# Kernel optimization log

Hardware: AMD Instinct MI355X
Metric: run time of the kernel (lower is better)

The kernel has to match this reference:

```python
import jax, jax.numpy as jnp
import numpy as np

DN = ('NCHW', 'OIHW', 'NCHW')

def conv(x, w, b, stride, pad):
    y = jax.lax.conv_general_dilated(x, w, (stride, stride), [(pad, pad), (pad, pad)], dimension_numbers=DN)
    return y if b is None else y + b[None, :, None, None]

def convT(x, w, b, stride, pad):
    # torch ConvTranspose2d weight layout: (in, out, kh, kw)
    wt = jnp.flip(w, (2, 3)).transpose(1, 0, 2, 3)
    p = w.shape[2] - 1 - pad
    y = jax.lax.conv_general_dilated(x, wt, (1, 1), [(p, p), (p, p)], lhs_dilation=(stride, stride), dimension_numbers=DN)
    return y + b[None, :, None, None]

def resblock(x, wa, wb):
    h = conv(jax.nn.relu(x), wa, None, 1, 1)   # 3x3, 128->32, no bias
    h = conv(jax.nn.relu(h), wb, None, 1, 0)   # 1x1, 32->128, no bias
    return x + h

def setup_inputs() -> dict:
    key = jax.random.key(0)
    ks = jax.random.split(key, 32)
    def w(i, shape):
        fan_in = int(np.prod(shape[1:]))
        return jax.random.normal(ks[i], shape, jnp.float32) * (1.0 / np.sqrt(fan_in))
    K, D = 512, 64
    inp = {
        'x':   jax.random.normal(ks[0], (16, 1, 256, 256), jnp.float32),
        'ew1': w(1, (64, 1, 4, 4)),    'eb1': jnp.zeros((64,), jnp.float32),
        'ew2': w(2, (128, 64, 4, 4)),  'eb2': jnp.zeros((128,), jnp.float32),
        'ew3': w(3, (128, 128, 3, 3)), 'eb3': jnp.zeros((128,), jnp.float32),
        'er1a': w(4, (32, 128, 3, 3)), 'er1b': w(5, (128, 32, 1, 1)),
        'er2a': w(6, (32, 128, 3, 3)), 'er2b': w(7, (128, 32, 1, 1)),
        'pw': w(8, (64, 128, 1, 1)),   'pb': jnp.zeros((64,), jnp.float32),
        'codebook': jax.random.uniform(ks[9], (K, D), jnp.float32, -1.0 / K, 1.0 / K),
        'dw1': w(10, (128, 64, 3, 3)), 'db1': jnp.zeros((128,), jnp.float32),
        'dr1a': w(11, (32, 128, 3, 3)), 'dr1b': w(12, (128, 32, 1, 1)),
        'dr2a': w(13, (32, 128, 3, 3)), 'dr2b': w(14, (128, 32, 1, 1)),
        'dtw1': w(15, (128, 64, 4, 4)), 'dtb1': jnp.zeros((64,), jnp.float32),  # ConvT: (in,out,kh,kw)
        'dtw2': w(16, (64, 1, 4, 4)),   'dtb2': jnp.zeros((1,), jnp.float32),
    }
    return inp

def vq(z, codebook, beta=0.25):
    zn = z.transpose(0, 2, 3, 1)                 # NHWC
    flat = zn.reshape(-1, codebook.shape[1])     # [N, D]
    d = jnp.sum(flat * flat, axis=1, keepdims=True) + jnp.sum(codebook * codebook, axis=1) - 2.0 * (flat @ codebook.T)  # [N, K]
    idx = jnp.argmin(d, axis=1)
    enc = jax.nn.one_hot(idx, codebook.shape[0], dtype=z.dtype)  # [N, K]
    q = codebook[idx].reshape(zn.shape)
    e_loss = jnp.mean(jnp.square(jax.lax.stop_gradient(q) - zn))
    q_loss = jnp.mean(jnp.square(q - jax.lax.stop_gradient(zn)))
    loss = q_loss + beta * e_loss
    q_st = zn + jax.lax.stop_gradient(q - zn)    # straight-through
    avg = jnp.mean(enc, axis=0)
    perplexity = jnp.exp(-jnp.sum(avg * jnp.log(avg + 1e-10)))
    return loss, q_st.transpose(0, 3, 1, 2), perplexity, enc

def reference(x, ew1, eb1, ew2, eb2, ew3, eb3, er1a, er1b, er2a, er2b, pw, pb, codebook, dw1, db1, dr1a, dr1b, dr2a, dr2b, dtw1, dtb1, dtw2, dtb2):
    # encoder
    h = jax.nn.relu(conv(x, ew1, eb1, 2, 1))
    h = jax.nn.relu(conv(h, ew2, eb2, 2, 1))
    h = conv(h, ew3, eb3, 1, 1)
    h = resblock(h, er1a, er1b)
    h = resblock(h, er2a, er2b)
    h = jax.nn.relu(h)
    z = conv(h, pw, pb, 1, 0)
    # vector quantizer
    loss, quantized, perplexity, encodings = vq(z, codebook)
    # decoder
    d = conv(quantized, dw1, db1, 1, 1)
    d = resblock(d, dr1a, dr1b)
    d = resblock(d, dr2a, dr2b)
    d = jax.nn.relu(convT(d, dtw1, dtb1, 2, 1))
    x_rec = convT(d, dtw2, dtb2, 2, 1)
    return (loss, x_rec, perplexity, encodings, quantized)
```

## Files before the change

### kernel.cpp

```cpp
#include <hip/hip_runtime.h>

#define TPB 256

typedef __attribute__((ext_vector_type(8))) short s8v;
typedef __attribute__((ext_vector_type(4))) float f4v;
typedef __bf16 bf16x8v __attribute__((ext_vector_type(8)));

__device__ inline short f2b(float f) {
    unsigned u = __builtin_bit_cast(unsigned, f);
    unsigned r = (u + 0x7FFF + ((u >> 16) & 1)) >> 16;
    return (short)r;
}
__device__ inline float b2f(short s) {
    unsigned u = ((unsigned)(unsigned short)s) << 16;
    return __builtin_bit_cast(float, u);
}
__device__ inline f4v mfma16(s8v a, s8v b, f4v c) {
    return __builtin_amdgcn_mfma_f32_16x16x32_bf16(
        __builtin_bit_cast(bf16x8v, a), __builtin_bit_cast(bf16x8v, b), c, 0, 0, 0);
}

struct WtDesc { const float* src; int CO, CI, T, iohw, start; };
struct WtArgs { WtDesc d[13]; int total; };

__global__ __launch_bounds__(256)
void wtall_k(WtArgs a, short* dst)
{
    int i = blockIdx.x * 256 + threadIdx.x;
    if (i >= a.total) return;
    int s = 0;
    for (int j = 1; j < 13; ++j) if (i >= a.d[j].start) s = j;
    int off = i - a.d[s].start;
    int CI = a.d[s].CI, CO = a.d[s].CO, T = a.d[s].T;
    int KC = CI >> 5, NT = CO >> 4;
    int j    = off & 7;
    int lane = (off >> 3) & 63;
    int rl = lane & 15, qd = lane >> 4;
    int blk = off >> 9;
    int nt  = blk % NT;
    int rest = blk / NT;
    int kc  = rest % KC;
    int tap = rest / KC;
    int co = nt * 16 + rl;
    int ci = kc * 32 + qd * 8 + j;
    float v = a.d[s].iohw ? a.d[s].src[(ci * CO + co) * T + tap]
                          : a.d[s].src[(co * CI + ci) * T + tap];
    dst[i] = f2b(v);
}

__global__ __launch_bounds__(256)
void cbprep_k(const float* __restrict__ cb, short* __restrict__ cbh,
              short* __restrict__ cbl, float* __restrict__ cbsq)
{
    int c = blockIdx.x * 256 + threadIdx.x;
    const float* src = cb + (size_t)c * 64;
    const int nt = c >> 4, rl = c & 15;
    float sq = 0.f;
    for (int d = 0; d < 64; ++d) {
        float v = src[d];
        sq += v * v;
        short h = f2b(v);
        short lo = f2b(v - b2f(h));
        int kc = d >> 5, qd = (d >> 3) & 3, j = d & 7;
        int pos = ((kc * 32 + nt) << 9) + ((qd * 16 + rl) << 3) + j;
        cbh[pos] = h;
        cbl[pos] = lo;
    }
    cbsq[c] = sq;
}

__global__ __launch_bounds__(256)
void conv1_k(const float* __restrict__ x, const float* __restrict__ w,
             const float* __restrict__ bias, short* __restrict__ out)
{
    __shared__ float sx[4 * 256];
    const int tid = threadIdx.x;
    const int oh = blockIdx.x, n = blockIdx.y;
    const int co = tid & 63, wv = tid >> 6;

    float wr[16];
#pragma unroll
    for (int t = 0; t < 16; ++t) wr[t] = w[co * 16 + t];
    const float b = bias[co];

    const float* xp = x + (size_t)n * 65536;
    for (int e = tid; e < 1024; e += 256) {
        int kh = e >> 8, col = e & 255;
        int ih = oh * 2 - 1 + kh;
        sx[e] = ((unsigned)ih < 256u) ? xp[ih * 256 + col] : 0.f;
    }
    __syncthreads();

    short* op = out + (((size_t)n * 128 + oh) * 128) * 64 + co;
#pragma unroll 4
    for (int i = 0; i < 32; ++i) {
        int ow = wv * 32 + i;
        int iwb = ow * 2 - 1;
        float acc = b;
#pragma unroll
        for (int kh = 0; kh < 4; ++kh) {
#pragma unroll
            for (int kw = 0; kw < 4; ++kw) {
                int iw = iwb + kw;
                float v = ((unsigned)iw < 256u) ? sx[kh * 256 + iw] : 0.f;
                acc = fmaf(v, wr[kh * 4 + kw], acc);
            }
        }
        op[(size_t)ow * 64] = f2b(fmaxf(acc, 0.f));
    }
}

template<int CI, int CO, bool RELU_IN, bool RELU_OUT, bool OUT_F32>
__global__ __launch_bounds__(256)
void pconv3s_k(const short* __restrict__ in, const short* __restrict__ wt,
               const float* __restrict__ bias, void* __restrict__ outv)
{
    constexpr int KC = CI / 32, NT = CO / 16;
    constexpr int NT2 = NT / 2;
    __shared__ short sA[3 * 66 * 40];

    const int tid = threadIdx.x;
    const int oh = blockIdx.x;
    const int n  = blockIdx.y;
    const short* inb = in + (size_t)n * 4096 * CI;
    const int w = tid >> 6, l = tid & 63, rl = l & 15, qd = l >> 4;
    const int mh = w & 1, nh = w >> 1;

    f4v acc[2][NT2];
#pragma unroll
    for (int a2 = 0; a2 < 2; ++a2)
#pragma unroll
        for (int nt = 0; nt < NT2; ++nt) acc[a2][nt] = (f4v)0.f;

    for (int kc = 0; kc < KC; ++kc) {
        __syncthreads();
        for (int e = tid; e < 792; e += 256) {
            int cell = e >> 2, kcn = e & 3;
            int hr = cell / 66, col = cell - hr * 66;
            int ih = oh - 1 + hr, iw = col - 1;
            s8v v = (s8v)0;
            if ((unsigned)ih < 64u && (unsigned)iw < 64u) {
                v = *(const s8v*)(inb + ((size_t)ih * 64 + iw) * CI + kc * 32 + kcn * 8);
                if (RELU_IN) {
#pragma unroll
                    for (int j = 0; j < 8; ++j) if (v[j] < (short)0) v[j] = 0;
                }
            }
            *(s8v*)&sA[(hr * 66 + col) * 40 + kcn * 8] = v;
        }
        __syncthreads();

#pragma unroll
        for (int tap = 0; tap < 9; ++tap) {
            const int kh = tap / 3, kw = tap % 3;
            s8v af[2];
#pragma unroll
            for (int a2 = 0; a2 < 2; ++a2)
                af[a2] = *(const s8v*)&sA[(kh * 66 + mh * 32 + a2 * 16 + rl + kw) * 40 + qd * 8];
            const short* wb = wt + (((size_t)(tap * KC + kc) * NT + nh * NT2) << 9) + l * 8;
#pragma unroll
            for (int nt = 0; nt < NT2; ++nt) {
                s8v b = *(const s8v*)(wb + ((size_t)nt << 9));
#pragma unroll
                for (int a2 = 0; a2 < 2; ++a2)
                    acc[a2][nt] = mfma16(af[a2], b, acc[a2][nt]);
            }
        }
    }

#pragma unroll
    for (int a2 = 0; a2 < 2; ++a2) {
#pragma unroll
        for (int rg = 0; rg < 4; ++rg) {
            int ow = mh * 32 + a2 * 16 + qd * 4 + rg;
            size_t row = (size_t)n * 4096 + (size_t)oh * 64 + ow;
#pragma unroll
            for (int nt = 0; nt < NT2; ++nt) {
                int co = nh * NT2 * 16 + nt * 16 + rl;
                float v = acc[a2][nt][rg];
                if (bias) v += bias[co];
                if (RELU_OUT) v = fmaxf(v, 0.f);
                if (OUT_F32) ((float*)outv)[row * CO + co] = v;
                else         ((short*)outv)[row * CO + co] = f2b(v);
            }
        }
    }
}

__global__ __launch_bounds__(256)
void rfuse_k(const short* __restrict__ in, const short* __restrict__ wa,
             const short* __restrict__ wb, short* __restrict__ out)
{
    __shared__ short sA[3 * 66 * 40];
    short* sMid = sA;

    const int tid = threadIdx.x;
    const int oh = blockIdx.x;
    const int n  = blockIdx.y;
    const short* inb = in + (size_t)n * 4096 * 128;
    const int w = tid >> 6, l = tid & 63, rl = l & 15, qd = l >> 4;

    f4v acc1[2];
    acc1[0] = (f4v)0.f; acc1[1] = (f4v)0.f;

    for (int kc = 0; kc < 4; ++kc) {
        __syncthreads();
        for (int e = tid; e < 792; e += 256) {
            int cell = e >> 2, kcn = e & 3;
            int hr = cell / 66, col = cell - hr * 66;
            int ih = oh - 1 + hr, iw = col - 1;
            s8v v = (s8v)0;
            if ((unsigned)ih < 64u && (unsigned)iw < 64u) {
                v = *(const s8v*)(inb + ((size_t)ih * 64 + iw) * 128 + kc * 32 + kcn * 8);
#pragma unroll
                for (int j = 0; j < 8; ++j) if (v[j] < (short)0) v[j] = 0;
            }
            *(s8v*)&sA[(hr * 66 + col) * 40 + kcn * 8] = v;
        }
        __syncthreads();

#pragma unroll
        for (int tap = 0; tap < 9; ++tap) {
            const int kh = tap / 3, kw = tap % 3;
            s8v af = *(const s8v*)&sA[(kh * 66 + w * 16 + rl + kw) * 40 + qd * 8];
            const short* wp = wa + (((size_t)(tap * 4 + kc) * 2) << 9) + l * 8;
            acc1[0] = mfma16(af, *(const s8v*)(wp),       acc1[0]);
            acc1[1] = mfma16(af, *(const s8v*)(wp + 512), acc1[1]);
        }
    }

    __syncthreads();
#pragma unroll
    for (int nt = 0; nt < 2; ++nt)
#pragma unroll
        for (int rg = 0; rg < 4; ++rg) {
            int m  = w * 16 + qd * 4 + rg;
            int co = nt * 16 + rl;
            sMid[m * 40 + co] = f2b(fmaxf(acc1[nt][rg], 0.f));
        }
    __syncthreads();

    f4v acc2[8];
#pragma unroll
    for (int nt = 0; nt < 8; ++nt) acc2[nt] = (f4v)0.f;

    s8v am = *(const s8v*)&sMid[(w * 16 + rl) * 40 + qd * 8];
#pragma unroll
    for (int nt = 0; nt < 8; ++nt) {
        s8v b = *(const s8v*)(wb + ((size_t)nt << 9) + l * 8);
        acc2[nt] = mfma16(am, b, acc2[nt]);
    }

    short* outb = out + (size_t)n * 4096 * 128;
    const size_t sp0 = (size_t)oh * 64;
#pragma unroll
    for (int rg = 0; rg < 4; ++rg) {
        int m = w * 16 + qd * 4 + rg;
        size_t sp = sp0 + m;
#pragma unroll
        for (int nt = 0; nt < 8; ++nt) {
            int co = nt * 16 + rl;
            float v = acc2[nt][rg] + b2f(inb[sp * 128 + co]);
            outb[sp * 128 + co] = f2b(v);
        }
    }
}

template<int CI, int CO, bool RELU_IN, bool RELU_OUT, bool OUT_F32>
__global__ __launch_bounds__(256)
void pconv1s_k(const short* __restrict__ in, const short* __restrict__ wt,
               const float* __restrict__ bias, void* __restrict__ outv)
{
    constexpr int KC = CI / 32, NT = CO / 16;
    __shared__ short sA[64 * 40];

    const int tid = threadIdx.x;
    const size_t r0 = (size_t)blockIdx.x * 64;
    const int w = tid >> 6, l = tid & 63, rl = l & 15, qd = l >> 4;

    f4v acc[NT];
#pragma unroll
    for (int nt = 0; nt < NT; ++nt) acc[nt] = (f4v)0.f;

    for (int kc = 0; kc < KC; ++kc) {
        __syncthreads();
        {
            int row = tid >> 2, kcn = tid & 3;
            s8v v = *(const s8v*)(in + (r0 + row) * CI + kc * 32 + kcn * 8);
            if (RELU_IN) {
#pragma unroll
                for (int j = 0; j < 8; ++j) if (v[j] < (short)0) v[j] = 0;
            }
            *(s8v*)&sA[row * 40 + kcn * 8] = v;
        }
        __syncthreads();

        s8v af = *(const s8v*)&sA[(w * 16 + rl) * 40 + qd * 8];
        const short* wb = wt + (((size_t)kc * NT) << 9) + l * 8;
#pragma unroll
        for (int nt = 0; nt < NT; ++nt) {
            s8v b = *(const s8v*)(wb + ((size_t)nt << 9));
            acc[nt] = mfma16(af, b, acc[nt]);
        }
    }

#pragma unroll
    for (int rg = 0; rg < 4; ++rg) {
        size_t row = r0 + w * 16 + qd * 4 + rg;
#pragma unroll
        for (int nt = 0; nt < NT; ++nt) {
            int co = nt * 16 + rl;
            float v = acc[nt][rg];
            if (bias) v += bias[co];
            if (RELU_OUT) v = fmaxf(v, 0.f);
            if (OUT_F32) ((float*)outv)[row * CO + co] = v;
            else         ((short*)outv)[row * CO + co] = f2b(v);
        }
    }
}

__global__ __launch_bounds__(256)
void pconv2_k(const short* __restrict__ in, const short* __restrict__ wt,
              const float* __restrict__ bias, short* __restrict__ out)
{
    __shared__ short sA[2 * 4 * 66 * 40];
    const int tid = threadIdx.x;
    const int oh = blockIdx.x, n = blockIdx.y;
    const short* inb = in + (size_t)n * 16384 * 64;
    const int w = tid >> 6, l = tid & 63, rl = l & 15, qd = l >> 4;
    const int mh = w & 1, nh = w >> 1;

    f4v acc[2][4];
#pragma unroll
    for (int a2 = 0; a2 < 2; ++a2)
#pragma unroll
        for (int nt = 0; nt < 4; ++nt) acc[a2][nt] = (f4v)0.f;

    for (int kc = 0; kc < 2; ++kc) {
        __syncthreads();
        for (int e = tid; e < 2112; e += 256) {
            int cell = e >> 2, kcn = e & 3;
            int par = cell / 264;
            int rem = cell - par * 264;
            int hr = rem / 66, c = rem - hr * 66;
            int iw = par ? (2 * c - 1) : (2 * c);
            int ih = oh * 2 - 1 + hr;
            s8v v = (s8v)0;
            if ((unsigned)ih < 128u && (unsigned)iw < 128u)
                v = *(const s8v*)(inb + ((size_t)ih * 128 + iw) * 64 + kc * 32 + kcn * 8);
            *(s8v*)&sA[((par * 4 + hr) * 66 + c) * 40 + kcn * 8] = v;
        }
        __syncthreads();

#pragma unroll
        for (int tap = 0; tap < 16; ++tap) {
            const int kh = tap >> 2, kw = tap & 3;
            const int par = 1 - (kw & 1), cofs = kw >> 1;
            s8v af[2];
#pragma unroll
            for (int a2 = 0; a2 < 2; ++a2) {
                int ow = mh * 32 + a2 * 16 + rl;
                af[a2] = *(const s8v*)&sA[((par * 4 + kh) * 66 + ow + cofs) * 40 + qd * 8];
            }
            const short* wb = wt + (((size_t)(tap * 2 + kc) * 8 + nh * 4) << 9) + l * 8;
#pragma unroll
            for (int nt = 0; nt < 4; ++nt) {
                s8v b = *(const s8v*)(wb + ((size_t)nt << 9));
#pragma unroll
                for (int a2 = 0; a2 < 2; ++a2)
                    acc[a2][nt] = mfma16(af[a2], b, acc[a2][nt]);
            }
        }
    }

#pragma unroll
    for (int a2 = 0; a2 < 2; ++a2) {
#pragma unroll
        for (int rg = 0; rg < 4; ++rg) {
            int ow = mh * 32 + a2 * 16 + qd * 4 + rg;
            size_t row = (size_t)n * 4096 + (size_t)oh * 64 + ow;
#pragma unroll
            for (int nt = 0; nt < 4; ++nt) {
                int co = nh * 64 + nt * 16 + rl;
                float v = acc[a2][nt][rg] + bias[co];
                out[row * 128 + co] = f2b(fmaxf(v, 0.f));
            }
        }
    }
}

__global__ __launch_bounds__(256)
void pct1_k(const short* __restrict__ in, const short* __restrict__ wt,
            const float* __restrict__ bias, short* __restrict__ out)
{
    __shared__ short sA[3 * 66 * 40];
    const int tid = threadIdx.x;
    const int bx = blockIdx.x, n = blockIdx.y;
    const int P = bx & 1;
    const int q2 = bx >> 1;
    const int oh0 = (q2 >> 1) * 4 + (q2 & 1);
    const int p = (oh0 + 1) & 1;
    const int ihb0 = (oh0 + 1 - p) >> 1;
    const short* inb = in + (size_t)n * 4096 * 128;
    const int w = tid >> 6, l = tid & 63, rl = l & 15, qd = l >> 4;
    const int mh = w & 1, nh = w >> 1;

    f4v acc[4][2];
#pragma unroll
    for (int a4 = 0; a4 < 4; ++a4)
#pragma unroll
        for (int nt = 0; nt < 2; ++nt) acc[a4][nt] = (f4v)0.f;

    for (int kc = 0; kc < 4; ++kc) {
        __syncthreads();
        for (int e = tid; e < 792; e += 256) {
            int cell = e >> 2, kcn = e & 3;
            int hr = cell / 66, c = cell - hr * 66;
            int ih = ihb0 - 1 + hr, iw = c - 1;
            s8v v = (s8v)0;
            if ((unsigned)ih < 64u && (unsigned)iw < 64u)
                v = *(const s8v*)(inb + ((size_t)ih * 64 + iw) * 128 + kc * 32 + kcn * 8);
            *(s8v*)&sA[(hr * 66 + c) * 40 + kcn * 8] = v;
        }
        __syncthreads();

#pragma unroll
        for (int a = 0; a < 2; ++a)
#pragma unroll
        for (int b = 0; b < 2; ++b) {
            const int kh = p + 2 * a;
            const int kw = (1 - P) + 2 * b;
            const int tap = kh * 4 + kw;
            const int hrw = mh + 1 - a;
            s8v af[4];
#pragma unroll
            for (int a4 = 0; a4 < 4; ++a4)
                af[a4] = *(const s8v*)&sA[(hrw * 66 + a4 * 16 + rl + P - b + 1) * 40 + qd * 8];
            const short* wbp = wt + (((size_t)(tap * 4 + kc) * 4 + nh * 2) << 9) + l * 8;
#pragma unroll
            for (int nt = 0; nt < 2; ++nt) {
                s8v bb = *(const s8v*)(wbp + ((size_t)nt << 9));
#pragma unroll
                for (int a4 = 0; a4 < 4; ++a4)
                    acc[a4][nt] = mfma16(af[a4], bb, acc[a4][nt]);
            }
        }
    }

#pragma unroll
    for (int a4 = 0; a4 < 4; ++a4) {
#pragma unroll
        for (int rg = 0; rg < 4; ++rg) {
            int j = a4 * 16 + qd * 4 + rg;
            int oh = oh0 + 2 * mh, ow = 2 * j + P;
            size_t pb = (((size_t)n * 128 + oh) * 128 + ow) * 64;
#pragma unroll
            for (int nt = 0; nt < 2; ++nt) {
                int co = nh * 32 + nt * 16 + rl;
                float v = acc[a4][nt][rg] + bias[co];
                out[pb + co] = f2b(fmaxf(v, 0.f));
            }
        }
    }
}

__global__ __launch_bounds__(256)
void convt2_k(const short* __restrict__ in, const float* __restrict__ w,
              const float* __restrict__ bias, float* __restrict__ out)
{
    __shared__ float sw[16 * 64];
    const int tid = threadIdx.x;
    for (int e = tid; e < 1024; e += 256) { int ci = e >> 4, tap = e & 15; sw[tap * 64 + ci] = w[e]; }
    __syncthreads();

    const int i = blockIdx.x * 256 + tid;
    const int n = i >> 16, s = i & 65535;
    const int oh = s >> 8, ow = s & 255;

    const int p = (oh + 1) & 1, q = (ow + 1) & 1;
    const int ihb = (oh + 1 - p) >> 1, iwb = (ow + 1 - q) >> 1;

    float acc = bias[0];
#pragma unroll
    for (int a = 0; a < 2; ++a) {
        int ih = ihb - a, kh = p + 2 * a;
        bool vr = (unsigned)ih < 128u;
#pragma unroll
        for (int b = 0; b < 2; ++b) {
            int iw = iwb - b, kw = q + 2 * b;
            if (vr && (unsigned)iw < 128u) {
                const short* ip = in + (((size_t)n * 128 + ih) * 128 + iw) * 64;
                const float* wp = &sw[(kh * 4 + kw) * 64];
#pragma unroll
                for (int c = 0; c < 64; c += 8) {
                    s8v v = *(const s8v*)(ip + c);
#pragma unroll
                    for (int j = 0; j < 8; ++j) acc += b2f(v[j]) * wp[c + j];
                }
            }
        }
    }
    out[i] = acc;
}

__global__ __launch_bounds__(256)
void vqm_k(const float* __restrict__ z, const short* __restrict__ cbh,
           const short* __restrict__ cbl, const float* __restrict__ cbsq,
           const float* __restrict__ cb,
           float* __restrict__ quant, short* __restrict__ qb,
           int* __restrict__ idxp, float* __restrict__ errbuf)
{
    __shared__ float zs[64 * 68];
    __shared__ short scb[2][8192];
    __shared__ int sidx[64];
    __shared__ float serr[4];
    float* qc = (float*)&scb[0][0];

    const int tid = threadIdx.x;
    const int w = tid >> 6, l = tid & 63, rl = l & 15, qd = l >> 4;
    const int r0 = blockIdx.x * 64;

    for (int e = tid; e < 1024; e += 256) {
        int row = e >> 4, c4 = e & 15;
        float4 t = ((const float4*)(z + (size_t)(r0 + row) * 64))[c4];
        *(float4*)&zs[row * 68 + c4 * 4] = t;
    }
    __syncthreads();

    s8v zh[2], zl[2];
#pragma unroll
    for (int kc = 0; kc < 2; ++kc) {
        const float* zp = &zs[(w * 16 + rl) * 68 + kc * 32 + qd * 8];
        s8v hi, lo;
#pragma unroll
        for (int j = 0; j < 8; ++j) {
            float v = zp[j];
            short h = f2b(v);
            hi[j] = h;
            lo[j] = f2b(v - b2f(h));
        }
        zh[kc] = hi; zl[kc] = lo;
    }

    float best[4]; int bidx[4];
#pragma unroll
    for (int rg = 0; rg < 4; ++rg) { best[rg] = 3.4e38f; bidx[rg] = 0; }

    for (int ch = 0; ch < 4; ++ch) {
        __syncthreads();
        for (int e = tid; e < 1024; e += 256) {
            int kcL = e >> 9, rest = e & 511;
            int ntl = rest >> 6, off = rest & 63;
            int srcIdx = (kcL * 32 + ch * 8 + ntl) * 64 + off;
            *(s8v*)&scb[0][e * 8] = ((const s8v*)cbh)[srcIdx];
            *(s8v*)&scb[1][e * 8] = ((const s8v*)cbl)[srcIdx];
        }
        __syncthreads();

        float sq[8];
#pragma unroll
        for (int nt = 0; nt < 8; ++nt) sq[nt] = cbsq[ch * 128 + nt * 16 + rl];

        f4v acc[8];
#pragma unroll
        for (int nt = 0; nt < 8; ++nt) acc[nt] = (f4v)0.f;
#pragma unroll
        for (int kc = 0; kc < 2; ++kc) {
#pragma unroll
            for (int nt = 0; nt < 8; ++nt) {
                s8v bh = *(const s8v*)&scb[0][(kc * 8 + nt) * 512 + l * 8];
                s8v bl = *(const s8v*)&scb[1][(kc * 8 + nt) * 512 + l * 8];
                acc[nt] = mfma16(zh[kc], bh, acc[nt]);
                acc[nt] = mfma16(zh[kc], bl, acc[nt]);
                acc[nt] = mfma16(zl[kc], bh, acc[nt]);
            }
        }

#pragma unroll
        for (int rg = 0; rg < 4; ++rg) {
            float bd = best[rg]; int bi = bidx[rg];
#pragma unroll
            for (int nt = 0; nt < 8; ++nt) {
                float d = sq[nt] - 2.f * acc[nt][rg];
                int code = ch * 128 + nt * 16 + rl;
                if (d < bd) { bd = d; bi = code; }
            }
            best[rg] = bd; bidx[rg] = bi;
        }
    }

#pragma unroll
    for (int rg = 0; rg < 4; ++rg) {
        float bd = best[rg]; int bi = bidx[rg];
#pragma unroll
        for (int off = 1; off < 16; off <<= 1) {
            float od = __shfl_xor(bd, off, 64);
            int   oi = __shfl_xor(bi, off, 64);
            if (od < bd || (od == bd && oi < bi)) { bd = od; bi = oi; }
        }
        if (rl == 0) sidx[w * 16 + qd * 4 + rg] = bi;
    }
    __syncthreads();

    const int n = r0 >> 12, s0 = r0 & 4095;
    float err = 0.f;
#pragma unroll 4
    for (int i = 0; i < 16; ++i) {
        int rr = w * 16 + i;
        int bi = sidx[rr];
        float c = cb[(size_t)bi * 64 + l];
        float zv = zs[rr * 68 + l];
        float dd = zv - c;
        err += dd * dd;
        qb[(size_t)(r0 + rr) * 64 + l] = f2b(c);
        qc[l * 68 + rr] = c;
    }
#pragma unroll
    for (int o = 32; o; o >>= 1) err += __shfl_down(err, o, 64);
    if (l == 0) serr[w] = err;
    if (tid < 64) idxp[r0 + tid] = sidx[tid];
    __syncthreads();

#pragma unroll 4
    for (int dd = 0; dd < 16; ++dd) {
        int d = w * 16 + dd;
        quant[((size_t)(n * 64 + d)) * 4096 + s0 + l] = qc[d * 68 + l];
    }
    if (tid == 0) errbuf[blockIdx.x] = serr[0] + serr[1] + serr[2] + serr[3];
}

__global__ __launch_bounds__(1024)
void fin_k(const int* __restrict__ idxp, const float* __restrict__ errbuf,
           float* out_loss, float* out_perp)
{
    __shared__ int lc[512];
    __shared__ float red[1024];
    const int t = threadIdx.x;
    if (t < 512) lc[t] = 0;
    __syncthreads();
    for (int i = t; i < 65536; i += 1024) atomicAdd(&lc[idxp[i]], 1);
    __syncthreads();
    float v = 0.f;
    if (t < 512) {
        float avg = (float)lc[t] * (1.0f / 65536.0f);
        v = avg * logf(avg + 1e-10f);
    }
    red[t] = v;
    __syncthreads();
    for (int st = 512; st; st >>= 1) { if (t < st) red[t] += red[t + st]; __syncthreads(); }
    if (t == 0) *out_perp = expf(-red[0]);
    __syncthreads();
    red[t] = errbuf[t];
    __syncthreads();
    for (int st = 512; st; st >>= 1) { if (t < st) red[t] += red[t + st]; __syncthreads(); }
    if (t == 0) *out_loss = red[0] * (1.25f / 4194304.0f);
}

__global__ __launch_bounds__(256)
void enc_k(const int* __restrict__ idxp, float4* __restrict__ enc)
{
    int i = blockIdx.x * 256 + threadIdx.x;
    int r = i >> 7, c4 = (i & 127) * 4;
    int k = idxp[r];
    float4 v;
    v.x = (k == c4)     ? 1.f : 0.f;
    v.y = (k == c4 + 1) ? 1.f : 0.f;
    v.z = (k == c4 + 2) ? 1.f : 0.f;
    v.w = (k == c4 + 3) ? 1.f : 0.f;
    enc[i] = v;
}

extern "C" void kernel_launch(void* const* d_in, const int* in_sizes, int n_in,
                              void* d_out, int out_size, void* d_ws, size_t ws_size,
                              hipStream_t stream)
{
    const float* x    = (const float*)d_in[0];
    const float* ew1  = (const float*)d_in[1];
    const float* eb1  = (const float*)d_in[2];
    const float* ew2  = (const float*)d_in[3];
    const float* eb2  = (const float*)d_in[4];
    const float* ew3  = (const float*)d_in[5];
    const float* eb3  = (const float*)d_in[6];
    const float* er1a = (const float*)d_in[7];
    const float* er1b = (const float*)d_in[8];
    const float* er2a = (const float*)d_in[9];
    const float* er2b = (const float*)d_in[10];
    const float* pw   = (const float*)d_in[11];
    const float* pb   = (const float*)d_in[12];
    const float* cb   = (const float*)d_in[13];
    const float* dw1w = (const float*)d_in[14];
    const float* db1  = (const float*)d_in[15];
    const float* dr1a = (const float*)d_in[16];
    const float* dr1b = (const float*)d_in[17];
    const float* dr2a = (const float*)d_in[18];
    const float* dr2b = (const float*)d_in[19];
    const float* dtw1 = (const float*)d_in[20];
    const float* dtb1 = (const float*)d_in[21];
    const float* dtw2 = (const float*)d_in[22];
    const float* dtb2 = (const float*)d_in[23];

    char* wsb = (char*)d_ws;
    short* wbase = (short*)wsb;
    short* wt2   = wbase;
    short* wt3   = wbase + 131072;
    short* wr1a  = wbase + 278528;
    short* wr1b  = wbase + 315392;
    short* wr2a  = wbase + 319488;
    short* wr2b  = wbase + 356352;
    short* wpwt  = wbase + 360448;
    short* wd1   = wbase + 368640;
    short* wdr1a = wbase + 442368;
    short* wdr1b = wbase + 479232;
    short* wdr2a = wbase + 483328;
    short* wdr2b = wbase + 520192;
    short* wtt1  = wbase + 524288;

    short* h2   = (short*)(wsb + 1310720);
    short* buf  = (short*)(wsb + 18087936);
    short* qb   = (short*)(wsb + 39059456);
    float* z    = (float*)(wsb + 47448064);
    int*   idx  = (int*)  (wsb + 64225280);
    if (ws_size < (size_t)64489480) return;

    float* out    = (float*)d_out;
    float* o_loss = out;
    float* xrec   = out + 1;
    float* o_perp = out + 1048577;
    float* enc    = out + 1048578;
    float* quant  = out + 34603010;
    char*  encB = (char*)d_out + (size_t)1048580 * 4;
    short* h1  = (short*)encB;
    short* dt1 = h1 + 16777216;
    short* cbh  = (short*)(encB + ((size_t)120 << 20));
    short* cbl  = cbh + 32768;
    float* cbsq = (float*)(cbl + 32768);
    float* errbuf = (float*)(encB + ((size_t)121 << 20));

    WtArgs wa;
    wa.d[0]  = { ew2,  128,  64, 16, 0, 0      };
    wa.d[1]  = { ew3,  128, 128,  9, 0, 131072 };
    wa.d[2]  = { er1a,  32, 128,  9, 0, 278528 };
    wa.d[3]  = { er1b, 128,  32,  1, 0, 315392 };
    wa.d[4]  = { er2a,  32, 128,  9, 0, 319488 };
    wa.d[5]  = { er2b, 128,  32,  1, 0, 356352 };
    wa.d[6]  = { pw,    64, 128,  1, 0, 360448 };
    wa.d[7]  = { dw1w, 128,  64,  9, 0, 368640 };
    wa.d[8]  = { dr1a,  32, 128,  9, 0, 442368 };
    wa.d[9]  = { dr1b, 128,  32,  1, 0, 479232 };
    wa.d[10] = { dr2a,  32, 128,  9, 0, 483328 };
    wa.d[11] = { dr2b, 128,  32,  1, 0, 520192 };
    wa.d[12] = { dtw1,  64, 128, 16, 1, 524288 };
    wa.total = 655360;
    wtall_k<<<dim3(2560), TPB, 0, stream>>>(wa, wbase);
    cbprep_k<<<dim3(2), TPB, 0, stream>>>(cb, cbh, cbl, cbsq);

    conv1_k<<<dim3(128, 16), TPB, 0, stream>>>(x, ew1, eb1, h1);
    pconv2_k<<<dim3(64, 16), TPB, 0, stream>>>(h1, wt2, eb2, h2);
    pconv3s_k<128,128,false,false,false><<<dim3(64,16), TPB, 0, stream>>>(h2, wt3, eb3, buf);
    rfuse_k<<<dim3(64,16), TPB, 0, stream>>>(buf, wr1a, wr1b, h2);
    rfuse_k<<<dim3(64,16), TPB, 0, stream>>>(h2,  wr2a, wr2b, buf);
    pconv1s_k<128, 64,true ,false,true ><<<dim3(1024), TPB, 0, stream>>>(buf, wpwt, pb, z);

    vqm_k<<<dim3(1024), TPB, 0, stream>>>(z, cbh, cbl, cbsq, cb, quant, qb, idx, errbuf);
    fin_k<<<dim3(1), 1024, 0, stream>>>(idx, errbuf, o_loss, o_perp);

    pconv3s_k< 64,128,false,false,false><<<dim3(64,16), TPB, 0, stream>>>(qb, wd1, db1, buf);
    rfuse_k<<<dim3(64,16), TPB, 0, stream>>>(buf, wdr1a, wdr1b, h2);
    rfuse_k<<<dim3(64,16), TPB, 0, stream>>>(h2,  wdr2a, wdr2b, buf);
    pct1_k<<<dim3(128, 16), TPB, 0, stream>>>(buf, wtt1, dtb1, dt1);
    convt2_k<<<dim3(4096), TPB, 0, stream>>>(dt1, dtw2, dtb2, xrec);

    enc_k<<<dim3(32768), TPB, 0, stream>>>(idx, (float4*)enc);
}
```

Baseline: 600.5 us.

## Fuse prep kernels, fold projection into resblock, swizzle block order, rework convT2

Merges the weight-repack and codebook-prep kernels into one launch. Fuses the final 1x1 projection conv (relu + pw + bias) into the second encoder residual block so the f32 z is written directly from it. Permutes block-to-row mapping in several conv kernels, which may improve cache locality across neighbouring rows. Rewrites the last transposed conv so each thread computes a 2x2 output quad from a shared 3x3 input neighbourhood, reusing loaded input and writing float2.

```diff
diff --git a/kernel.cpp b/kernel.cpp
--- a/kernel.cpp
+++ b/kernel.cpp
@@ -24,9 +24,30 @@
 struct WtArgs { WtDesc d[13]; int total; };
 
 __global__ __launch_bounds__(256)
-void wtall_k(WtArgs a, short* dst)
-{
-    int i = blockIdx.x * 256 + threadIdx.x;
+void prep_k(WtArgs a, short* dst, const float* __restrict__ cb,
+            short* __restrict__ cbh, short* __restrict__ cbl, float* __restrict__ cbsq)
+{
+    const int bx = blockIdx.x;
+    const int tid = threadIdx.x;
+    if (bx >= 2560) {
+        int c = (bx - 2560) * 256 + tid;
+        const float* src = cb + (size_t)c * 64;
+        const int nt = c >> 4, rl = c & 15;
+        float sq = 0.f;
+        for (int d = 0; d < 64; ++d) {
+            float v = src[d];
+            sq += v * v;
+            short h = f2b(v);
+            short lo = f2b(v - b2f(h));
+            int kc = d >> 5, qd = (d >> 3) & 3, j = d & 7;
+            int pos = ((kc * 32 + nt) << 9) + ((qd * 16 + rl) << 3) + j;
+            cbh[pos] = h;
+            cbl[pos] = lo;
+        }
+        cbsq[c] = sq;
+        return;
+    }
+    int i = bx * 256 + tid;
     if (i >= a.total) return;
     int s = 0;
     for (int j = 1; j < 13; ++j) if (i >= a.d[j].start) s = j;
@@ -49,33 +70,14 @@
 }
 
 __global__ __launch_bounds__(256)
-void cbprep_k(const float* __restrict__ cb, short* __restrict__ cbh,
-              short* __restrict__ cbl, float* __restrict__ cbsq)
-{
-    int c = blockIdx.x * 256 + threadIdx.x;
-    const float* src = cb + (size_t)c * 64;
-    const int nt = c >> 4, rl = c & 15;
-    float sq = 0.f;
-    for (int d = 0; d < 64; ++d) {
-        float v = src[d];
-        sq += v * v;
-        short h = f2b(v);
-        short lo = f2b(v - b2f(h));
-        int kc = d >> 5, qd = (d >> 3) & 3, j = d & 7;
-        int pos = ((kc * 32 + nt) << 9) + ((qd * 16 + rl) << 3) + j;
-        cbh[pos] = h;
-        cbl[pos] = lo;
-    }
-    cbsq[c] = sq;
-}
-
-__global__ __launch_bounds__(256)
 void conv1_k(const float* __restrict__ x, const float* __restrict__ w,
              const float* __restrict__ bias, short* __restrict__ out)
 {
     __shared__ float sx[4 * 256];
     const int tid = threadIdx.x;
-    const int oh = blockIdx.x, n = blockIdx.y;
+    const int bx = blockIdx.x;
+    const int oh = ((bx & 7) << 4) | (bx >> 3);
+    const int n = blockIdx.y;
     const int co = tid & 63, wv = tid >> 6;
 
     float wr[16];
@@ -120,7 +122,8 @@
     __shared__ short sA[3 * 66 * 40];
 
     const int tid = threadIdx.x;
-    const int oh = blockIdx.x;
+    const int bx = blockIdx.x;
+    const int oh = ((bx & 7) << 3) | (bx >> 3);
     const int n  = blockIdx.y;
     const short* inb = in + (size_t)n * 4096 * CI;
     const int w = tid >> 6, l = tid & 63, rl = l & 15, qd = l >> 4;
@@ -187,15 +190,21 @@
     }
 }
 
+template<int Z>
 __global__ __launch_bounds__(256)
 void rfuse_k(const short* __restrict__ in, const short* __restrict__ wa,
-             const short* __restrict__ wb, short* __restrict__ out)
-{
-    __shared__ short sA[3 * 66 * 40];
-    short* sMid = sA;
+             const short* __restrict__ wb, short* __restrict__ out,
+             const short* __restrict__ wz, const float* __restrict__ zb,
+             float* __restrict__ zout)
+{
+    __shared__ short smem[8704];
+    short* sA = smem;
+    short* sMid = smem;
+    short* sZ = smem;
 
     const int tid = threadIdx.x;
-    const int oh = blockIdx.x;
+    const int bx = blockIdx.x;
+    const int oh = ((bx & 7) << 3) | (bx >> 3);
     const int n  = blockIdx.y;
     const short* inb = in + (size_t)n * 4096 * 128;
     const int w = tid >> 6, l = tid & 63, rl = l & 15, qd = l >> 4;
@@ -251,70 +260,58 @@
         acc2[nt] = mfma16(am, b, acc2[nt]);
     }
 
-    short* outb = out + (size_t)n * 4096 * 128;
     const size_t sp0 = (size_t)oh * 64;
-#pragma unroll
-    for (int rg = 0; rg < 4; ++rg) {
-        int m = w * 16 + qd * 4 + rg;
-        size_t sp = sp0 + m;
-#pragma unroll
-        for (int nt = 0; nt < 8; ++nt) {
-            int co = nt * 16 + rl;
-            float v = acc2[nt][rg] + b2f(inb[sp * 128 + co]);
-            outb[sp * 128 + co] = f2b(v);
-        }
-    }
-}
-
-template<int CI, int CO, bool RELU_IN, bool RELU_OUT, bool OUT_F32>
-__global__ __launch_bounds__(256)
-void pconv1s_k(const short* __restrict__ in, const short* __restrict__ wt,
-               const float* __restrict__ bias, void* __restrict__ outv)
-{
-    constexpr int KC = CI / 32, NT = CO / 16;
-    __shared__ short sA[64 * 40];
-
-    const int tid = threadIdx.x;
-    const size_t r0 = (size_t)blockIdx.x * 64;
-    const int w = tid >> 6, l = tid & 63, rl = l & 15, qd = l >> 4;
-
-    f4v acc[NT];
-#pragma unroll
-    for (int nt = 0; nt < NT; ++nt) acc[nt] = (f4v)0.f;
-
-    for (int kc = 0; kc < KC; ++kc) {
-        __syncthreads();
-        {
-            int row = tid >> 2, kcn = tid & 3;
-            s8v v = *(const s8v*)(in + (r0 + row) * CI + kc * 32 + kcn * 8);
-            if (RELU_IN) {
-#pragma unroll
-                for (int j = 0; j < 8; ++j) if (v[j] < (short)0) v[j] = 0;
-            }
-            *(s8v*)&sA[row * 40 + kcn * 8] = v;
-        }
-        __syncthreads();
-
-        s8v af = *(const s8v*)&sA[(w * 16 + rl) * 40 + qd * 8];
-        const short* wb = wt + (((size_t)kc * NT) << 9) + l * 8;
-#pragma unroll
-        for (int nt = 0; nt < NT; ++nt) {
-            s8v b = *(const s8v*)(wb + ((size_t)nt << 9));
-            acc[nt] = mfma16(af, b, acc[nt]);
-        }
-    }
-
-#pragma unroll
-    for (int rg = 0; rg < 4; ++rg) {
-        size_t row = r0 + w * 16 + qd * 4 + rg;
-#pragma unroll
-        for (int nt = 0; nt < NT; ++nt) {
-            int co = nt * 16 + rl;
-            float v = acc[nt][rg];
-            if (bias) v += bias[co];
-            if (RELU_OUT) v = fmaxf(v, 0.f);
-            if (OUT_F32) ((float*)outv)[row * CO + co] = v;
-            else         ((short*)outv)[row * CO + co] = f2b(v);
+    if (Z == 0) {
+        short* outb = out + (size_t)n * 4096 * 128;
+#pragma unroll
+        for (int rg = 0; rg < 4; ++rg) {
+            int m = w * 16 + qd * 4 + rg;
+            size_t sp = sp0 + m;
+#pragma unroll
+            for (int nt = 0; nt < 8; ++nt) {
+                int co = nt * 16 + rl;
+                float v = acc2[nt][rg] + b2f(inb[sp * 128 + co]);
+                outb[sp * 128 + co] = f2b(v);
+            }
+        }
+    } else {
+        __syncthreads();
+#pragma unroll
+        for (int rg = 0; rg < 4; ++rg) {
+            int m = w * 16 + qd * 4 + rg;
+            size_t sp = sp0 + m;
+#pragma unroll
+            for (int nt = 0; nt < 8; ++nt) {
+                int co = nt * 16 + rl;
+                float v = acc2[nt][rg] + b2f(inb[sp * 128 + co]);
+                sZ[m * 136 + co] = f2b(fmaxf(v, 0.f));
+            }
+        }
+        __syncthreads();
+
+        f4v acc3[4];
+#pragma unroll
+        for (int nt = 0; nt < 4; ++nt) acc3[nt] = (f4v)0.f;
+        s8v am2[4];
+#pragma unroll
+        for (int kc = 0; kc < 4; ++kc)
+            am2[kc] = *(const s8v*)&sZ[(w * 16 + rl) * 136 + kc * 32 + qd * 8];
+#pragma unroll
+        for (int kc = 0; kc < 4; ++kc)
+#pragma unroll
+            for (int nt = 0; nt < 4; ++nt) {
+                s8v b = *(const s8v*)(wz + (((size_t)(kc * 4 + nt)) << 9) + l * 8);
+                acc3[nt] = mfma16(am2[kc], b, acc3[nt]);
+            }
+        const size_t zr0 = (size_t)n * 4096 + (size_t)oh * 64;
+#pragma unroll
+        for (int rg = 0; rg < 4; ++rg) {
+            size_t row = zr0 + w * 16 + qd * 4 + rg;
+#pragma unroll
+            for (int nt = 0; nt < 4; ++nt) {
+                int co = nt * 16 + rl;
+                zout[row * 64 + co] = acc3[nt][rg] + zb[co];
+            }
         }
     }
 }
@@ -325,7 +322,9 @@
 {
     __shared__ short sA[2 * 4 * 66 * 40];
     const int tid = threadIdx.x;
-    const int oh = blockIdx.x, n = blockIdx.y;
+    const int bx = blockIdx.x;
+    const int oh = ((bx & 7) << 3) | (bx >> 3);
+    const int n = blockIdx.y;
     const short* inb = in + (size_t)n * 16384 * 64;
     const int w = tid >> 6, l = tid & 63, rl = l & 15, qd = l >> 4;
     const int mh = w & 1, nh = w >> 1;
@@ -396,8 +395,9 @@
     __shared__ short sA[3 * 66 * 40];
     const int tid = threadIdx.x;
     const int bx = blockIdx.x, n = blockIdx.y;
-    const int P = bx & 1;
-    const int q2 = bx >> 1;
+    const int k8 = bx & 7;
+    const int P  = (bx >> 3) & 1;
+    const int q2 = k8 * 8 + (bx >> 4);
     const int oh0 = (q2 >> 1) * 4 + (q2 & 1);
     const int p = (oh0 + 1) & 1;
     const int ihb0 = (oh0 + 1 - p) >> 1;
@@ -473,34 +473,60 @@
     for (int e = tid; e < 1024; e += 256) { int ci = e >> 4, tap = e & 15; sw[tap * 64 + ci] = w[e]; }
     __syncthreads();
 
-    const int i = blockIdx.x * 256 + tid;
-    const int n = i >> 16, s = i & 65535;
-    const int oh = s >> 8, ow = s & 255;
-
-    const int p = (oh + 1) & 1, q = (ow + 1) & 1;
-    const int ihb = (oh + 1 - p) >> 1, iwb = (ow + 1 - q) >> 1;
-
-    float acc = bias[0];
-#pragma unroll
-    for (int a = 0; a < 2; ++a) {
-        int ih = ihb - a, kh = p + 2 * a;
-        bool vr = (unsigned)ih < 128u;
-#pragma unroll
-        for (int b = 0; b < 2; ++b) {
-            int iw = iwb - b, kw = q + 2 * b;
-            if (vr && (unsigned)iw < 128u) {
-                const short* ip = in + (((size_t)n * 128 + ih) * 128 + iw) * 64;
-                const float* wp = &sw[(kh * 4 + kw) * 64];
-#pragma unroll
-                for (int c = 0; c < 64; c += 8) {
-                    s8v v = *(const s8v*)(ip + c);
-#pragma unroll
-                    for (int j = 0; j < 8; ++j) acc += b2f(v[j]) * wp[c + j];
+    const int bx = blockIdx.x, n = blockIdx.y;
+    const int qpair = ((bx & 7) << 3) | (bx >> 3);
+    const int i = qpair * 2 + (tid >> 7);
+    const int j = tid & 127;
+    const short* inb = in + (size_t)n * 16384 * 64;
+    const float b0 = bias[0];
+
+    float acc[2][2] = {{b0, b0}, {b0, b0}};
+
+#pragma unroll
+    for (int cc = 0; cc < 8; ++cc) {
+        s8v iv[3][3];
+#pragma unroll
+        for (int r = 0; r < 3; ++r) {
+            int ih = i - 1 + r;
+            bool vr = (unsigned)ih < 128u;
+#pragma unroll
+            for (int c3 = 0; c3 < 3; ++c3) {
+                int iw = j - 1 + c3;
+                iv[r][c3] = (vr && (unsigned)iw < 128u)
+                    ? *(const s8v*)(inb + ((size_t)ih * 128 + iw) * 64 + cc * 8)
+                    : (s8v)0;
+            }
+        }
+#pragma unroll
+        for (int e = 0; e < 8; ++e) {
+            int ci = cc * 8 + e;
+            float fv[3][3];
+#pragma unroll
+            for (int r = 0; r < 3; ++r)
+#pragma unroll
+                for (int c3 = 0; c3 < 3; ++c3) fv[r][c3] = b2f(iv[r][c3][e]);
+#pragma unroll
+            for (int dy = 0; dy < 2; ++dy)
+#pragma unroll
+            for (int dx = 0; dx < 2; ++dx) {
+#pragma unroll
+                for (int a = 0; a < 2; ++a)
+#pragma unroll
+                for (int b = 0; b < 2; ++b) {
+                    int tap = ((1 - dy) + 2 * a) * 4 + (1 - dx) + 2 * b;
+                    acc[dy][dx] = fmaf(fv[dy + 1 - a][dx + 1 - b], sw[tap * 64 + ci], acc[dy][dx]);
                 }
             }
         }
     }
-    out[i] = acc;
+
+    float* ob = out + (size_t)n * 65536;
+#pragma unroll
+    for (int dy = 0; dy < 2; ++dy) {
+        int oh = 2 * i + dy;
+        float2 v; v.x = acc[dy][0]; v.y = acc[dy][1];
+        *(float2*)&ob[(size_t)oh * 256 + 2 * j] = v;
+    }
 }
 
 __global__ __launch_bounds__(256)
@@ -751,24 +777,22 @@
     wa.d[11] = { dr2b, 128,  32,  1, 0, 520192 };
     wa.d[12] = { dtw1,  64, 128, 16, 1, 524288 };
     wa.total = 655360;
-    wtall_k<<<dim3(2560), TPB, 0, stream>>>(wa, wbase);
-    cbprep_k<<<dim3(2), TPB, 0, stream>>>(cb, cbh, cbl, cbsq);
+    prep_k<<<dim3(2562), TPB, 0, stream>>>(wa, wbase, cb, cbh, cbl, cbsq);
 
     conv1_k<<<dim3(128, 16), TPB, 0, stream>>>(x, ew1, eb1, h1);
     pconv2_k<<<dim3(64, 16), TPB, 0, stream>>>(h1, wt2, eb2, h2);
     pconv3s_k<128,128,false,false,false><<<dim3(64,16), TPB, 0, stream>>>(h2, wt3, eb3, buf);
-    rfuse_k<<<dim3(64,16), TPB, 0, stream>>>(buf, wr1a, wr1b, h2);
-    rfuse_k<<<dim3(64,16), TPB, 0, stream>>>(h2,  wr2a, wr2b, buf);
-    pconv1s_k<128, 64,true ,false,true ><<<dim3(1024), TPB, 0, stream>>>(buf, wpwt, pb, z);
+    rfuse_k<0><<<dim3(64,16), TPB, 0, stream>>>(buf, wr1a, wr1b, h2, nullptr, nullptr, nullptr);
+    rfuse_k<1><<<dim3(64,16), TPB, 0, stream>>>(h2,  wr2a, wr2b, nullptr, wpwt, pb, z);
 
     vqm_k<<<dim3(1024), TPB, 0, stream>>>(z, cbh, cbl, cbsq, cb, quant, qb, idx, errbuf);
     fin_k<<<dim3(1), 1024, 0, stream>>>(idx, errbuf, o_loss, o_perp);
 
     pconv3s_k< 64,128,false,false,false><<<dim3(64,16), TPB, 0, stream>>>(qb, wd1, db1, buf);
-    rfuse_k<<<dim3(64,16), TPB, 0, stream>>>(buf, wdr1a, wdr1b, h2);
-    rfuse_k<<<dim3(64,16), TPB, 0, stream>>>(h2,  wdr2a, wdr2b, buf);
+    rfuse_k<0><<<dim3(64,16), TPB, 0, stream>>>(buf, wdr1a, wdr1b, h2, nullptr, nullptr, nullptr);
+    rfuse_k<0><<<dim3(64,16), TPB, 0, stream>>>(h2,  wdr2a, wdr2b, buf, nullptr, nullptr, nullptr);
     pct1_k<<<dim3(128, 16), TPB, 0, stream>>>(buf, wtt1, dtb1, dt1);
-    convt2_k<<<dim3(4096), TPB, 0, stream>>>(dt1, dtw2, dtb2, xrec);
+    convt2_k<<<dim3(64, 16), TPB, 0, stream>>>(dt1, dtw2, dtb2, xrec);
 
     enc_k<<<dim3(32768), TPB, 0, stream>>>(idx, (float4*)enc);
 }
```

Measured after the change: 948.0 us. +57.9%, slower.
